# Kernel optimization log

Hardware: AMD Instinct MI355X
Metric: run time of the kernel (lower is better)

The kernel has to match this reference:

```python
import jax, jax.numpy as jnp
import numpy as np

N_NODES = 40000
N_EDGES = 640000
IN_CH = 128
OUT_CH = 128
NUM_RBF = 64


def setup_inputs() -> dict:
    key = jax.random.key(0)
    ks = jax.random.split(key, 8)
    x = jax.random.normal(ks[0], (N_NODES, IN_CH), dtype=jnp.float32)
    edge_index = jax.random.randint(ks[1], (2, N_EDGES), 0, N_NODES, dtype=jnp.int64)
    edge_rbf = jax.random.uniform(ks[2], (N_EDGES, NUM_RBF), dtype=jnp.float32)
    s1 = 1.0 / np.sqrt(NUM_RBF)
    s2 = 1.0 / np.sqrt(OUT_CH)
    sl = 1.0 / np.sqrt(IN_CH)
    W1 = jax.random.normal(ks[3], (NUM_RBF, OUT_CH), dtype=jnp.float32) * s1
    b1 = jnp.zeros((OUT_CH,), dtype=jnp.float32)
    W2 = jax.random.normal(ks[4], (OUT_CH, OUT_CH), dtype=jnp.float32) * s2
    b2 = jnp.zeros((OUT_CH,), dtype=jnp.float32)
    Wl = jax.random.normal(ks[5], (IN_CH, OUT_CH), dtype=jnp.float32) * sl
    bl = jnp.zeros((OUT_CH,), dtype=jnp.float32)
    return {"x": x, "edge_index": edge_index, "edge_rbf": edge_rbf,
            "W1": W1, "b1": b1, "W2": W2, "b2": b2, "Wl": Wl, "bl": bl}


def reference(x, edge_index, edge_rbf, W1, b1, W2, b2, Wl, bl):
    # filter_net: Linear -> ReLU -> Linear on edge RBF features  [E, OUT_CH]
    weight = jnp.maximum(edge_rbf @ W1 + b1, 0.0) @ W2 + b2
    # node linear projection  [N, OUT_CH]
    h = x @ Wl + bl
    row, col = edge_index[0], edge_index[1]
    # gather source node features, modulate by continuous filter
    msg = h[col] * weight  # [E, OUT_CH]
    # scatter-sum messages onto destination nodes
    out = jax.ops.segment_sum(msg, row, num_segments=x.shape[0])
    return out
```

## Files before the change

kernel.cpp:

```cpp
#include <hip/hip_runtime.h>


#define N_NODES 40000
#define N_EDGES 640000
#define IN_CH 128
#define OUT_CH 128
#define NUM_RBF 64

#define TILE_M 64
#define NTILES (N_EDGES / TILE_M)
#define NB_NODE (N_NODES / TILE_M)
#define RBF_STR 72
#define T_STR 136
#define HV_STR 136
#define W1_STR 72
#define W2_STR 136
#define NSCB ((N_NODES + 255) / 256)
#define EDGE_GRID 1024
#define K1_GRID 1024
#define ZC_BLOCKS 32

typedef __attribute__((ext_vector_type(8))) short bf16x8;
typedef __attribute__((ext_vector_type(16))) float f32x16;

__device__ __forceinline__ unsigned short f2bf(float f) {
  unsigned u = __float_as_uint(f);
  return (unsigned short)((u + 0x7FFFu + ((u >> 16) & 1u)) >> 16);
}
__device__ __forceinline__ float bf2f(unsigned short s) {
  return __uint_as_float(((unsigned)s) << 16);
}

__global__ __launch_bounds__(256) void k1_kernel(
    const float* __restrict__ x, const float* __restrict__ Wl,
    const float* __restrict__ bl, unsigned short* __restrict__ hbf,
    int* __restrict__ count, float* __restrict__ outp) {
  __shared__ __align__(16) char pool[IN_CH * W2_STR * 2];
  const int bid = blockIdx.x;
  const int t = threadIdx.x;

  if (bid >= NB_NODE) {
    if (bid < NB_NODE + ZC_BLOCKS) {
      if (count) {
        int4 z = {0, 0, 0, 0};
        for (int i = (bid - NB_NODE) * 256 + t; i < N_NODES / 4;
             i += ZC_BLOCKS * 256)
          ((int4*)count)[i] = z;
      }
    } else {
      if (outp) {
        float4 z = {0.f, 0.f, 0.f, 0.f};
        const int nb = K1_GRID - NB_NODE - ZC_BLOCKS;
        for (int i = (bid - NB_NODE - ZC_BLOCKS) * 256 + t;
             i < N_NODES * OUT_CH / 4; i += nb * 256)
          ((float4*)outp)[i] = z;
      }
    }
    return;
  }

  const int lane = t & 63;
  const int l31 = lane & 31;
  const int lhalf = lane >> 5;
  const int wv = t >> 6;
  const int nbase = wv * 32 + l31;

  {
    unsigned short* sWT = (unsigned short*)pool;
    const int k2 = t >> 1;
    const int d0 = (t & 1) * 64;
#pragma unroll
    for (int i = 0; i < 16; ++i) {
      float4 v = *(const float4*)(Wl + k2 * OUT_CH + d0 + 4 * i);
      sWT[(d0 + 4 * i + 0) * W2_STR + k2] = f2bf(v.x);
      sWT[(d0 + 4 * i + 1) * W2_STR + k2] = f2bf(v.y);
      sWT[(d0 + 4 * i + 2) * W2_STR + k2] = f2bf(v.z);
      sWT[(d0 + 4 * i + 3) * W2_STR + k2] = f2bf(v.w);
    }
  }
  __syncthreads();
  bf16x8 BW[8];
  {
    const unsigned short* sWT = (const unsigned short*)pool;
#pragma unroll
    for (int kk = 0; kk < 8; ++kk)
      BW[kk] = *(const bf16x8*)&sWT[nbase * W2_STR + kk * 16 + lhalf * 8];
  }
  const float blv = bl[nbase];
  __syncthreads();

  const int rbase = bid * TILE_M;
  unsigned short* sX = (unsigned short*)pool;
  {
    const int m = t >> 2;
    const int c0 = (t & 3) * 32;
    const float* src = x + (size_t)(rbase + m) * IN_CH + c0;
#pragma unroll
    for (int i = 0; i < 8; ++i) {
      float4 v = *(const float4*)(src + 4 * i);
      ushort4 p;
      p.x = f2bf(v.x); p.y = f2bf(v.y); p.z = f2bf(v.z); p.w = f2bf(v.w);
      *(ushort4*)&sX[m * T_STR + c0 + 4 * i] = p;
    }
  }
  __syncthreads();
#pragma unroll
  for (int mt = 0; mt < 2; ++mt) {
    f32x16 acc = {0.f, 0.f, 0.f, 0.f, 0.f, 0.f, 0.f, 0.f,
                  0.f, 0.f, 0.f, 0.f, 0.f, 0.f, 0.f, 0.f};
#pragma unroll
    for (int kk = 0; kk < 8; ++kk) {
      bf16x8 A = *(const bf16x8*)&sX[(mt * 32 + l31) * T_STR + kk * 16 + lhalf * 8];
      acc = __builtin_amdgcn_mfma_f32_32x32x16_bf16(A, BW[kk], acc, 0, 0, 0);
    }
#pragma unroll
    for (int r = 0; r < 16; ++r) {
      const int rowm = mt * 32 + (r & 3) + 8 * (r >> 2) + 4 * lhalf;
      hbf[(size_t)(rbase + rowm) * OUT_CH + nbase] = f2bf(acc[r] + blv);
    }
  }
}

__global__ void hist_kernel(const int* __restrict__ rowI, int* __restrict__ count,
                            unsigned long long* __restrict__ status) {
  if (blockIdx.x == 0 && threadIdx.x < NSCB) status[threadIdx.x] = 0ULL;
  int e = blockIdx.x * 256 + threadIdx.x;
  if (e < N_EDGES) atomicAdd(&count[rowI[e]], 1);
}

__global__ __launch_bounds__(256) void scan_kernel(
    const int* __restrict__ count, unsigned long long* __restrict__ status,
    int* __restrict__ cursor) {
  __shared__ int s[256];
  __shared__ int wsum[4];
  const int t = threadIdx.x;
  const int b = blockIdx.x;
  const int i = b * 256 + t;
  const int v = (i < N_NODES) ? count[i] : 0;
  s[t] = v;
  __syncthreads();
  for (int off = 1; off < 256; off <<= 1) {
    int u = (t >= off) ? s[t - off] : 0;
    __syncthreads();
    s[t] += u;
    __syncthreads();
  }
  if (t == 255)
    __hip_atomic_store(&status[b], (1ULL << 32) | (unsigned)s[255],
                       __ATOMIC_RELEASE, __HIP_MEMORY_SCOPE_AGENT);
  int contrib = 0;
  if (t < b) {
    unsigned long long sv;
    do {
      sv = __hip_atomic_load(&status[t], __ATOMIC_ACQUIRE,
                             __HIP_MEMORY_SCOPE_AGENT);
    } while (!(sv >> 32));
    contrib = (int)(unsigned)sv;
  }
  for (int o = 32; o > 0; o >>= 1) contrib += __shfl_down(contrib, o, 64);
  if ((t & 63) == 0) wsum[t >> 6] = contrib;
  __syncthreads();
  const int boffv = wsum[0] + wsum[1] + wsum[2] + wsum[3];
  if (i < N_NODES) cursor[i] = boffv + s[t] - v;
}

__global__ void scatter_kernel(const int* __restrict__ rowI,
                               const int* __restrict__ colI,
                               int* __restrict__ cursor,
                               unsigned long long* __restrict__ packed) {
  int e = blockIdx.x * 256 + threadIdx.x;
  if (e < N_EDGES) {
    const int r = rowI[e];
    const int c = colI[e];
    const int p = atomicAdd(&cursor[r], 1);
    packed[p] = ((unsigned long long)r << 36) | ((unsigned long long)c << 20) |
                (unsigned)e;
  }
}

__global__ __launch_bounds__(256, 3) void edge_fused_kernel(
    const unsigned long long* __restrict__ packed, const float* __restrict__ rbf,
    const float* __restrict__ W1, const float* __restrict__ b1,
    const float* __restrict__ W2, const float* __restrict__ b2,
    const unsigned short* __restrict__ hbf, float* __restrict__ outp) {
  __shared__ __align__(16) char pool[IN_CH * W2_STR * 2];

  unsigned short* sHv = (unsigned short*)pool;
  unsigned short* sT = (unsigned short*)pool;
  unsigned short* sRbf = (unsigned short*)(pool + TILE_M * HV_STR * 2);
  int* sAux = (int*)(pool + TILE_M * HV_STR * 2 + TILE_M * RBF_STR * 2);

  const int t = threadIdx.x;
  const int lane = t & 63;
  const int l31 = lane & 31;
  const int lhalf = lane >> 5;
  const int wv = t >> 6;
  const int nbase = wv * 32 + l31;

  {
    unsigned short* sW1T = (unsigned short*)pool;
    const int k = t >> 2;
    const int c0 = (t & 3) * 32;
#pragma unroll
    for (int i = 0; i < 8; ++i) {
      float4 v = *(const float4*)(W1 + k * OUT_CH + c0 + 4 * i);
      sW1T[(c0 + 4 * i + 0) * W1_STR + k] = f2bf(v.x);
      sW1T[(c0 + 4 * i + 1) * W1_STR + k] = f2bf(v.y);
      sW1T[(c0 + 4 * i + 2) * W1_STR + k] = f2bf(v.z);
      sW1T[(c0 + 4 * i + 3) * W1_STR + k] = f2bf(v.w);
    }
  }
  __syncthreads();
  bf16x8 B1[4];
  {
    const unsigned short* sW1T = (const unsigned short*)pool;
#pragma unroll
    for (int kk = 0; kk < 4; ++kk)
      B1[kk] = *(const bf16x8*)&sW1T[nbase * W1_STR + kk * 16 + lhalf * 8];
  }
  __syncthreads();
  {
    unsigned short* sW2T = (unsigned short*)pool;
    const int k2 = t >> 1;
    const int d0 = (t & 1) * 64;
#pragma unroll
    for (int i = 0; i < 16; ++i) {
      float4 v = *(const float4*)(W2 + k2 * OUT_CH + d0 + 4 * i);
      sW2T[(d0 + 4 * i + 0) * W2_STR + k2] = f2bf(v.x);
      sW2T[(d0 + 4 * i + 1) * W2_STR + k2] = f2bf(v.y);
      sW2T[(d0 + 4 * i + 2) * W2_STR + k2] = f2bf(v.z);
      sW2T[(d0 + 4 * i + 3) * W2_STR + k2] = f2bf(v.w);
    }
  }
  __syncthreads();
  bf16x8 B2[8];
  {
    const unsigned short* sW2T = (const unsigned short*)pool;
#pragma unroll
    for (int kk = 0; kk < 8; ++kk)
      B2[kk] = *(const bf16x8*)&sW2T[nbase * W2_STR + kk * 16 + lhalf * 8];
  }
  const float b1v = b1[nbase];
  const float b2v = b2[nbase];

  const int m4 = t >> 2;
  const int kq = (t & 3) * 16;
  const int rrow = t >> 4;
  const int c8 = (t & 15) * 8;

  float4 rb0, rb1, rb2, rb3;
  uint4 hq0, hq1, hq2, hq3;
  int auxv = 0;

#define PREFETCH(EB)                                                          \
  do {                                                                        \
    const unsigned long long pkm = packed[(EB) + m4];                         \
    const float* psrc = rbf + (size_t)(pkm & 0xFFFFFu) * NUM_RBF + kq;        \
    rb0 = *(const float4*)(psrc + 0);                                         \
    rb1 = *(const float4*)(psrc + 4);                                         \
    rb2 = *(const float4*)(psrc + 8);                                         \
    rb3 = *(const float4*)(psrc + 12);                                        \
    hq0 = *(const uint4*)(hbf +                                               \
        (size_t)((packed[(EB) + 0 + rrow] >> 20) & 0xFFFFu) * OUT_CH + c8);   \
    hq1 = *(const uint4*)(hbf +                                               \
        (size_t)((packed[(EB) + 16 + rrow] >> 20) & 0xFFFFu) * OUT_CH + c8);  \
    hq2 = *(const uint4*)(hbf +                                               \
        (size_t)((packed[(EB) + 32 + rrow] >> 20) & 0xFFFFu) * OUT_CH + c8);  \
    hq3 = *(const uint4*)(hbf +                                               \
        (size_t)((packed[(EB) + 48 + rrow] >> 20) & 0xFFFFu) * OUT_CH + c8);  \
    if (t < TILE_M) auxv = (int)(packed[(EB) + t] >> 36);                     \
  } while (0)

  int tile = blockIdx.x;
  if (tile < NTILES) PREFETCH(tile * TILE_M);

  for (; tile < NTILES; tile += gridDim.x) {
    __syncthreads();

    {
      ushort4 p;
      p.x = f2bf(rb0.x); p.y = f2bf(rb0.y); p.z = f2bf(rb0.z); p.w = f2bf(rb0.w);
      *(ushort4*)&sRbf[m4 * RBF_STR + kq + 0] = p;
      p.x = f2bf(rb1.x); p.y = f2bf(rb1.y); p.z = f2bf(rb1.z); p.w = f2bf(rb1.w);
      *(ushort4*)&sRbf[m4 * RBF_STR + kq + 4] = p;
      p.x = f2bf(rb2.x); p.y = f2bf(rb2.y); p.z = f2bf(rb2.z); p.w = f2bf(rb2.w);
      *(ushort4*)&sRbf[m4 * RBF_STR + kq + 8] = p;
      p.x = f2bf(rb3.x); p.y = f2bf(rb3.y); p.z = f2bf(rb3.z); p.w = f2bf(rb3.w);
      *(ushort4*)&sRbf[m4 * RBF_STR + kq + 12] = p;
    }
    *(uint4*)&sHv[(rrow + 0) * HV_STR + c8] = hq0;
    *(uint4*)&sHv[(rrow + 16) * HV_STR + c8] = hq1;
    *(uint4*)&sHv[(rrow + 32) * HV_STR + c8] = hq2;
    *(uint4*)&sHv[(rrow + 48) * HV_STR + c8] = hq3;
    if (t < TILE_M) sAux[t] = auxv;
    __syncthreads();

    const int tn = tile + gridDim.x;
    if (tn < NTILES) PREFETCH(tn * TILE_M);

    float hv[2][16];
#pragma unroll
    for (int mt = 0; mt < 2; ++mt)
#pragma unroll
      for (int r = 0; r < 16; ++r) {
        const int rowm = mt * 32 + (r & 3) + 8 * (r >> 2) + 4 * lhalf;
        hv[mt][r] = bf2f(sHv[rowm * HV_STR + nbase]);
      }
    __syncthreads();

#pragma unroll
    for (int mt = 0; mt < 2; ++mt) {
      f32x16 acc = {0.f, 0.f, 0.f, 0.f, 0.f, 0.f, 0.f, 0.f,
                    0.f, 0.f, 0.f, 0.f, 0.f, 0.f, 0.f, 0.f};
#pragma unroll
      for (int kk = 0; kk < 4; ++kk) {
        bf16x8 A = *(const bf16x8*)&sRbf[(mt * 32 + l31) * RBF_STR + kk * 16 + lhalf * 8];
        acc = __builtin_amdgcn_mfma_f32_32x32x16_bf16(A, B1[kk], acc, 0, 0, 0);
      }
#pragma unroll
      for (int r = 0; r < 16; ++r) {
        const int rowm = (r & 3) + 8 * (r >> 2) + 4 * lhalf;
        float v = acc[r] + b1v;
        v = v > 0.f ? v : 0.f;
        sT[(mt * 32 + rowm) * T_STR + nbase] = f2bf(v);
      }
    }
    __syncthreads();

    float sum = 0.f;
    int curd = -1;
#pragma unroll
    for (int mt = 0; mt < 2; ++mt) {
      f32x16 acc = {0.f, 0.f, 0.f, 0.f, 0.f, 0.f, 0.f, 0.f,
                    0.f, 0.f, 0.f, 0.f, 0.f, 0.f, 0.f, 0.f};
#pragma unroll
      for (int kk = 0; kk < 8; ++kk) {
        bf16x8 A = *(const bf16x8*)&sT[(mt * 32 + l31) * T_STR + kk * 16 + lhalf * 8];
        acc = __builtin_amdgcn_mfma_f32_32x32x16_bf16(A, B2[kk], acc, 0, 0, 0);
      }
#pragma unroll
      for (int r = 0; r < 16; ++r) {
        const int rowm = mt * 32 + (r & 3) + 8 * (r >> 2) + 4 * lhalf;
        const float m = hv[mt][r] * (acc[r] + b2v);
        const int d = sAux[rowm];
        if (d != curd) {
          if (curd >= 0) atomicAdd(&outp[(size_t)curd * OUT_CH + nbase], sum);
          curd = d;
          sum = m;
        } else {
          sum += m;
        }
      }
    }
    atomicAdd(&outp[(size_t)curd * OUT_CH + nbase], sum);
  }
#undef PREFETCH
}

__global__ __launch_bounds__(256, 3) void edge_atomic_kernel(
    const int* __restrict__ eidx, const float* __restrict__ rbf,
    const float* __restrict__ W1, const float* __restrict__ b1,
    const float* __restrict__ W2, const float* __restrict__ b2,
    const unsigned short* __restrict__ hbf, float* __restrict__ outp) {
  __shared__ __align__(16) char pool[IN_CH * W2_STR * 2];

  unsigned short* sHv = (unsigned short*)pool;
  unsigned short* sT = (unsigned short*)pool;
  unsigned short* sRbf = (unsigned short*)(pool + TILE_M * HV_STR * 2);
  int* sAux = (int*)(pool + TILE_M * HV_STR * 2 + TILE_M * RBF_STR * 2);

  const int t = threadIdx.x;
  const int lane = t & 63;
  const int l31 = lane & 31;
  const int lhalf = lane >> 5;
  const int wv = t >> 6;
  const int nbase = wv * 32 + l31;

  {
    unsigned short* sW1T = (unsigned short*)pool;
    const int k = t >> 2;
    const int c0 = (t & 3) * 32;
#pragma unroll
    for (int i = 0; i < 8; ++i) {
      float4 v = *(const float4*)(W1 + k * OUT_CH + c0 + 4 * i);
      sW1T[(c0 + 4 * i + 0) * W1_STR + k] = f2bf(v.x);
      sW1T[(c0 + 4 * i + 1) * W1_STR + k] = f2bf(v.y);
      sW1T[(c0 + 4 * i + 2) * W1_STR + k] = f2bf(v.z);
      sW1T[(c0 + 4 * i + 3) * W1_STR + k] = f2bf(v.w);
    }
  }
  __syncthreads();
  bf16x8 B1[4];
  {
    const unsigned short* sW1T = (const unsigned short*)pool;
#pragma unroll
    for (int kk = 0; kk < 4; ++kk)
      B1[kk] = *(const bf16x8*)&sW1T[nbase * W1_STR + kk * 16 + lhalf * 8];
  }
  __syncthreads();
  {
    unsigned short* sW2T = (unsigned short*)pool;
    const int k2 = t >> 1;
    const int d0 = (t & 1) * 64;
#pragma unroll
    for (int i = 0; i < 16; ++i) {
      float4 v = *(const float4*)(W2 + k2 * OUT_CH + d0 + 4 * i);
      sW2T[(d0 + 4 * i + 0) * W2_STR + k2] = f2bf(v.x);
      sW2T[(d0 + 4 * i + 1) * W2_STR + k2] = f2bf(v.y);
      sW2T[(d0 + 4 * i + 2) * W2_STR + k2] = f2bf(v.z);
      sW2T[(d0 + 4 * i + 3) * W2_STR + k2] = f2bf(v.w);
    }
  }
  __syncthreads();
  bf16x8 B2[8];
  {
    const unsigned short* sW2T = (const unsigned short*)pool;
#pragma unroll
    for (int kk = 0; kk < 8; ++kk)
      B2[kk] = *(const bf16x8*)&sW2T[nbase * W2_STR + kk * 16 + lhalf * 8];
  }
  const float b1v = b1[nbase];
  const float b2v = b2[nbase];

  const int* rowI = eidx;
  const int* colI = eidx + N_EDGES;

  for (int tile = blockIdx.x; tile < NTILES; tile += gridDim.x) {
    const int ebase = tile * TILE_M;
    __syncthreads();
    {
      const int m = t >> 2;
      const int kq = (t & 3) * 16;
      const float* src = rbf + (size_t)(ebase + m) * NUM_RBF + kq;
#pragma unroll
      for (int i = 0; i < 4; ++i) {
        float4 v = *(const float4*)(src + 4 * i);
        ushort4 p;
        p.x = f2bf(v.x); p.y = f2bf(v.y); p.z = f2bf(v.z); p.w = f2bf(v.w);
        *(ushort4*)&sRbf[m * RBF_STR + kq + 4 * i] = p;
      }
#pragma unroll
      for (int i = 0; i < 4; ++i) {
        const int chunk = t + 256 * i;
        const int row = chunk >> 4;
        const int c8 = (chunk & 15) * 8;
        const int col = colI[ebase + row];
        *(uint4*)&sHv[row * HV_STR + c8] =
            *(const uint4*)(hbf + (size_t)col * OUT_CH + c8);
      }
      if (t < TILE_M) sAux[t] = rowI[ebase + t];
    }
    __syncthreads();

    float hv[2][16];
#pragma unroll
    for (int mt = 0; mt < 2; ++mt)
#pragma unroll
      for (int r = 0; r < 16; ++r) {
        const int rowm = mt * 32 + (r & 3) + 8 * (r >> 2) + 4 * lhalf;
        hv[mt][r] = bf2f(sHv[rowm * HV_STR + nbase]);
      }
    __syncthreads();

#pragma unroll
    for (int mt = 0; mt < 2; ++mt) {
      f32x16 acc = {0.f, 0.f, 0.f, 0.f, 0.f, 0.f, 0.f, 0.f,
                    0.f, 0.f, 0.f, 0.f, 0.f, 0.f, 0.f, 0.f};
#pragma unroll
      for (int kk = 0; kk < 4; ++kk) {
        bf16x8 A = *(const bf16x8*)&sRbf[(mt * 32 + l31) * RBF_STR + kk * 16 + lhalf * 8];
        acc = __builtin_amdgcn_mfma_f32_32x32x16_bf16(A, B1[kk], acc, 0, 0, 0);
      }
#pragma unroll
      for (int r = 0; r < 16; ++r) {
        const int rowm = (r & 3) + 8 * (r >> 2) + 4 * lhalf;
        float v = acc[r] + b1v;
        v = v > 0.f ? v : 0.f;
        sT[(mt * 32 + rowm) * T_STR + nbase] = f2bf(v);
      }
    }
    __syncthreads();

    float sum = 0.f;
    int curd = -1;
#pragma unroll
    for (int mt = 0; mt < 2; ++mt) {
      f32x16 acc = {0.f, 0.f, 0.f, 0.f, 0.f, 0.f, 0.f, 0.f,
                    0.f, 0.f, 0.f, 0.f, 0.f, 0.f, 0.f, 0.f};
#pragma unroll
      for (int kk = 0; kk < 8; ++kk) {
        bf16x8 A = *(const bf16x8*)&sT[(mt * 32 + l31) * T_STR + kk * 16 + lhalf * 8];
        acc = __builtin_amdgcn_mfma_f32_32x32x16_bf16(A, B2[kk], acc, 0, 0, 0);
      }
#pragma unroll
      for (int r = 0; r < 16; ++r) {
        const int rowm = mt * 32 + (r & 3) + 8 * (r >> 2) + 4 * lhalf;
        const float m = hv[mt][r] * (acc[r] + b2v);
        const int d = sAux[rowm];
        if (d != curd) {
          if (curd >= 0) atomicAdd(&outp[(size_t)curd * OUT_CH + nbase], sum);
          curd = d;
          sum = m;
        } else {
          sum += m;
        }
      }
    }
    atomicAdd(&outp[(size_t)curd * OUT_CH + nbase], sum);
  }
}

extern "C" void kernel_launch(void* const* d_in, const int* in_sizes, int n_in,
                              void* d_out, int out_size, void* d_ws, size_t ws_size,
                              hipStream_t stream) {
  const float* x    = (const float*)d_in[0];
  const int*   eidx = (const int*)d_in[1];
  const float* rbf  = (const float*)d_in[2];
  const float* W1   = (const float*)d_in[3];
  const float* b1   = (const float*)d_in[4];
  const float* W2   = (const float*)d_in[5];
  const float* b2   = (const float*)d_in[6];
  const float* Wl   = (const float*)d_in[7];
  const float* bl   = (const float*)d_in[8];
  float* out = (float*)d_out;

  char* ws = (char*)d_ws;
  const size_t HBF_B = (size_t)N_NODES * OUT_CH * 2;
  const size_t PK_B = (size_t)N_EDGES * 8;
  const size_t CNT_B = (size_t)N_NODES * 4;
  const size_t ST_B = 1280;
  const size_t need = HBF_B + PK_B + 2 * CNT_B + ST_B + 64;

  size_t off = 0;
  unsigned short* hbf = (unsigned short*)(ws + off); off += HBF_B;
  unsigned long long* packed = (unsigned long long*)(ws + off); off += PK_B;
  int* count  = (int*)(ws + off); off += CNT_B;
  int* cursor = (int*)(ws + off); off += CNT_B;
  unsigned long long* status = (unsigned long long*)(ws + off); off += ST_B;

  const int* rowI = eidx;
  const int* colI = eidx + N_EDGES;

  if (ws_size >= need) {
    k1_kernel<<<K1_GRID, 256, 0, stream>>>(x, Wl, bl, hbf, count, out);
    hist_kernel<<<(N_EDGES + 255) / 256, 256, 0, stream>>>(rowI, count, status);
    scan_kernel<<<NSCB, 256, 0, stream>>>(count, status, cursor);
    scatter_kernel<<<(N_EDGES + 255) / 256, 256, 0, stream>>>(
        rowI, colI, cursor, packed);
    edge_fused_kernel<<<EDGE_GRID, 256, 0, stream>>>(
        packed, rbf, W1, b1, W2, b2, hbf, out);
  } else {
    hipMemsetAsync(out, 0, (size_t)N_NODES * OUT_CH * sizeof(float), stream);
    k1_kernel<<<NB_NODE, 256, 0, stream>>>(x, Wl, bl, hbf, nullptr, nullptr);
    edge_atomic_kernel<<<EDGE_GRID, 256, 0, stream>>>(
        eidx, rbf, W1, b1, W2, b2, hbf, out);
  }
}
```

Measured before the change: 418.8 us.

## Fold histogram into node-projection kernel and split packed edge keys into arrays

```diff
diff --git a/kernel.cpp b/kernel.cpp
--- a/kernel.cpp
+++ b/kernel.cpp
@@ -9,7 +9,7 @@
 
 #define TILE_M 64
 #define NTILES (N_EDGES / TILE_M)
-#define NB_NODE (N_NODES / TILE_M)
+#define NB_NODE (N_NODES / 64)
 #define RBF_STR 72
 #define T_STR 136
 #define HV_STR 136
@@ -18,7 +18,6 @@
 #define NSCB ((N_NODES + 255) / 256)
 #define EDGE_GRID 1024
 #define K1_GRID 1024
-#define ZC_BLOCKS 32
 
 typedef __attribute__((ext_vector_type(8))) short bf16x8;
 typedef __attribute__((ext_vector_type(16))) float f32x16;
@@ -34,27 +33,23 @@
 __global__ __launch_bounds__(256) void k1_kernel(
     const float* __restrict__ x, const float* __restrict__ Wl,
     const float* __restrict__ bl, unsigned short* __restrict__ hbf,
-    int* __restrict__ count, float* __restrict__ outp) {
+    const int* __restrict__ rowI, int* __restrict__ count,
+    float* __restrict__ outp) {
   __shared__ __align__(16) char pool[IN_CH * W2_STR * 2];
   const int bid = blockIdx.x;
   const int t = threadIdx.x;
 
   if (bid >= NB_NODE) {
-    if (bid < NB_NODE + ZC_BLOCKS) {
-      if (count) {
-        int4 z = {0, 0, 0, 0};
-        for (int i = (bid - NB_NODE) * 256 + t; i < N_NODES / 4;
-             i += ZC_BLOCKS * 256)
-          ((int4*)count)[i] = z;
-      }
-    } else {
-      if (outp) {
-        float4 z = {0.f, 0.f, 0.f, 0.f};
-        const int nb = K1_GRID - NB_NODE - ZC_BLOCKS;
-        for (int i = (bid - NB_NODE - ZC_BLOCKS) * 256 + t;
-             i < N_NODES * OUT_CH / 4; i += nb * 256)
-          ((float4*)outp)[i] = z;
-      }
+    const int nb = K1_GRID - NB_NODE;
+    if (outp) {
+      float4 z = {0.f, 0.f, 0.f, 0.f};
+      for (int i = (bid - NB_NODE) * 256 + t; i < N_NODES * OUT_CH / 4;
+           i += nb * 256)
+        ((float4*)outp)[i] = z;
+    }
+    if (count) {
+      for (int e = (bid - NB_NODE) * 256 + t; e < N_EDGES; e += nb * 256)
+        atomicAdd(&count[rowI[e]], 1);
     }
     return;
   }
@@ -89,7 +84,7 @@
   const float blv = bl[nbase];
   __syncthreads();
 
-  const int rbase = bid * TILE_M;
+  const int rbase = bid * 64;
   unsigned short* sX = (unsigned short*)pool;
   {
     const int m = t >> 2;
@@ -119,13 +114,6 @@
       hbf[(size_t)(rbase + rowm) * OUT_CH + nbase] = f2bf(acc[r] + blv);
     }
   }
-}
-
-__global__ void hist_kernel(const int* __restrict__ rowI, int* __restrict__ count,
-                            unsigned long long* __restrict__ status) {
-  if (blockIdx.x == 0 && threadIdx.x < NSCB) status[threadIdx.x] = 0ULL;
-  int e = blockIdx.x * 256 + threadIdx.x;
-  if (e < N_EDGES) atomicAdd(&count[rowI[e]], 1);
 }
 
 __global__ __launch_bounds__(256) void scan_kernel(
@@ -167,22 +155,24 @@
 __global__ void scatter_kernel(const int* __restrict__ rowI,
                                const int* __restrict__ colI,
                                int* __restrict__ cursor,
-                               unsigned long long* __restrict__ packed) {
+                               int* __restrict__ eperm, int* __restrict__ dsts,
+                               int* __restrict__ cols) {
   int e = blockIdx.x * 256 + threadIdx.x;
   if (e < N_EDGES) {
     const int r = rowI[e];
-    const int c = colI[e];
     const int p = atomicAdd(&cursor[r], 1);
-    packed[p] = ((unsigned long long)r << 36) | ((unsigned long long)c << 20) |
-                (unsigned)e;
-  }
-}
-
-__global__ __launch_bounds__(256, 3) void edge_fused_kernel(
-    const unsigned long long* __restrict__ packed, const float* __restrict__ rbf,
+    eperm[p] = e;
+    dsts[p] = r;
+    cols[p] = colI[e];
+  }
+}
+
+__global__ __launch_bounds__(256, 4) void edge_fused_kernel(
+    const int* __restrict__ eperm, const float* __restrict__ rbf,
     const float* __restrict__ W1, const float* __restrict__ b1,
     const float* __restrict__ W2, const float* __restrict__ b2,
-    const unsigned short* __restrict__ hbf, float* __restrict__ outp) {
+    const unsigned short* __restrict__ hbf, const int* __restrict__ dsts,
+    const int* __restrict__ cols, float* __restrict__ outp) {
   __shared__ __align__(16) char pool[IN_CH * W2_STR * 2];
 
   unsigned short* sHv = (unsigned short*)pool;
@@ -245,36 +235,22 @@
 
   const int m4 = t >> 2;
   const int kq = (t & 3) * 16;
-  const int rrow = t >> 4;
-  const int c8 = (t & 15) * 8;
 
   float4 rb0, rb1, rb2, rb3;
-  uint4 hq0, hq1, hq2, hq3;
-  int auxv = 0;
-
-#define PREFETCH(EB)                                                          \
-  do {                                                                        \
-    const unsigned long long pkm = packed[(EB) + m4];                         \
-    const float* psrc = rbf + (size_t)(pkm & 0xFFFFFu) * NUM_RBF + kq;        \
-    rb0 = *(const float4*)(psrc + 0);                                         \
-    rb1 = *(const float4*)(psrc + 4);                                         \
-    rb2 = *(const float4*)(psrc + 8);                                         \
-    rb3 = *(const float4*)(psrc + 12);                                        \
-    hq0 = *(const uint4*)(hbf +                                               \
-        (size_t)((packed[(EB) + 0 + rrow] >> 20) & 0xFFFFu) * OUT_CH + c8);   \
-    hq1 = *(const uint4*)(hbf +                                               \
-        (size_t)((packed[(EB) + 16 + rrow] >> 20) & 0xFFFFu) * OUT_CH + c8);  \
-    hq2 = *(const uint4*)(hbf +                                               \
-        (size_t)((packed[(EB) + 32 + rrow] >> 20) & 0xFFFFu) * OUT_CH + c8);  \
-    hq3 = *(const uint4*)(hbf +                                               \
-        (size_t)((packed[(EB) + 48 + rrow] >> 20) & 0xFFFFu) * OUT_CH + c8);  \
-    if (t < TILE_M) auxv = (int)(packed[(EB) + t] >> 36);                     \
+#define ISSUE_RBF(EB)                                                   \
+  do {                                                                  \
+    const int ep_ = eperm[(EB) + m4];                                   \
+    const float* ps_ = rbf + (size_t)ep_ * NUM_RBF + kq;                \
+    rb0 = *(const float4*)(ps_ + 0);                                    \
+    rb1 = *(const float4*)(ps_ + 4);                                    \
+    rb2 = *(const float4*)(ps_ + 8);                                    \
+    rb3 = *(const float4*)(ps_ + 12);                                   \
   } while (0)
 
-  int tile = blockIdx.x;
-  if (tile < NTILES) PREFETCH(tile * TILE_M);
-
-  for (; tile < NTILES; tile += gridDim.x) {
+  ISSUE_RBF(blockIdx.x * TILE_M);
+
+  for (int tile = blockIdx.x; tile < NTILES; tile += gridDim.x) {
+    const int ebase = tile * TILE_M;
     __syncthreads();
 
     {
@@ -287,16 +263,18 @@
       *(ushort4*)&sRbf[m4 * RBF_STR + kq + 8] = p;
       p.x = f2bf(rb3.x); p.y = f2bf(rb3.y); p.z = f2bf(rb3.z); p.w = f2bf(rb3.w);
       *(ushort4*)&sRbf[m4 * RBF_STR + kq + 12] = p;
-    }
-    *(uint4*)&sHv[(rrow + 0) * HV_STR + c8] = hq0;
-    *(uint4*)&sHv[(rrow + 16) * HV_STR + c8] = hq1;
-    *(uint4*)&sHv[(rrow + 32) * HV_STR + c8] = hq2;
-    *(uint4*)&sHv[(rrow + 48) * HV_STR + c8] = hq3;
-    if (t < TILE_M) sAux[t] = auxv;
-    __syncthreads();
-
-    const int tn = tile + gridDim.x;
-    if (tn < NTILES) PREFETCH(tn * TILE_M);
+#pragma unroll
+      for (int i = 0; i < 4; ++i) {
+        const int chunk = t + 256 * i;
+        const int row = chunk >> 4;
+        const int c8 = (chunk & 15) * 8;
+        const int col = cols[ebase + row];
+        *(uint4*)&sHv[row * HV_STR + c8] =
+            *(const uint4*)(hbf + (size_t)col * OUT_CH + c8);
+      }
+      if (t < TILE_M) sAux[t] = dsts[ebase + t];
+    }
+    __syncthreads();
 
     float hv[2][16];
 #pragma unroll
@@ -326,6 +304,9 @@
       }
     }
     __syncthreads();
+
+    const int tn = tile + gridDim.x;
+    if (tn < NTILES) ISSUE_RBF(tn * TILE_M);
 
     float sum = 0.f;
     int curd = -1;
@@ -354,10 +335,10 @@
     }
     atomicAdd(&outp[(size_t)curd * OUT_CH + nbase], sum);
   }
-#undef PREFETCH
-}
-
-__global__ __launch_bounds__(256, 3) void edge_atomic_kernel(
+#undef ISSUE_RBF
+}
+
+__global__ __launch_bounds__(256, 4) void edge_atomic_kernel(
     const int* __restrict__ eidx, const float* __restrict__ rbf,
     const float* __restrict__ W1, const float* __restrict__ b1,
     const float* __restrict__ W2, const float* __restrict__ b2,
@@ -526,32 +507,35 @@
 
   char* ws = (char*)d_ws;
   const size_t HBF_B = (size_t)N_NODES * OUT_CH * 2;
-  const size_t PK_B = (size_t)N_EDGES * 8;
+  const size_t EP_B = (size_t)N_EDGES * 4;
   const size_t CNT_B = (size_t)N_NODES * 4;
   const size_t ST_B = 1280;
-  const size_t need = HBF_B + PK_B + 2 * CNT_B + ST_B + 64;
+  const size_t need = HBF_B + 3 * EP_B + 2 * CNT_B + ST_B + 64;
 
   size_t off = 0;
   unsigned short* hbf = (unsigned short*)(ws + off); off += HBF_B;
-  unsigned long long* packed = (unsigned long long*)(ws + off); off += PK_B;
-  int* count  = (int*)(ws + off); off += CNT_B;
+  int* eperm = (int*)(ws + off); off += EP_B;
+  int* dsts  = (int*)(ws + off); off += EP_B;
+  int* cols  = (int*)(ws + off); off += EP_B;
+  int* count = (int*)(ws + off); off += CNT_B;
+  unsigned long long* status = (unsigned long long*)(ws + off); off += ST_B;
   int* cursor = (int*)(ws + off); off += CNT_B;
-  unsigned long long* status = (unsigned long long*)(ws + off); off += ST_B;
 
   const int* rowI = eidx;
   const int* colI = eidx + N_EDGES;
 
   if (ws_size >= need) {
-    k1_kernel<<<K1_GRID, 256, 0, stream>>>(x, Wl, bl, hbf, count, out);
-    hist_kernel<<<(N_EDGES + 255) / 256, 256, 0, stream>>>(rowI, count, status);
+    hipMemsetAsync(count, 0, CNT_B + ST_B, stream);
+    k1_kernel<<<K1_GRID, 256, 0, stream>>>(x, Wl, bl, hbf, rowI, count, out);
     scan_kernel<<<NSCB, 256, 0, stream>>>(count, status, cursor);
     scatter_kernel<<<(N_EDGES + 255) / 256, 256, 0, stream>>>(
-        rowI, colI, cursor, packed);
+        rowI, colI, cursor, eperm, dsts, cols);
     edge_fused_kernel<<<EDGE_GRID, 256, 0, stream>>>(
-        packed, rbf, W1, b1, W2, b2, hbf, out);
+        eperm, rbf, W1, b1, W2, b2, hbf, dsts, cols, out);
   } else {
     hipMemsetAsync(out, 0, (size_t)N_NODES * OUT_CH * sizeof(float), stream);
-    k1_kernel<<<NB_NODE, 256, 0, stream>>>(x, Wl, bl, hbf, nullptr, nullptr);
+    k1_kernel<<<NB_NODE, 256, 0, stream>>>(x, Wl, bl, hbf, rowI, nullptr,
+                                           nullptr);
     edge_atomic_kernel<<<EDGE_GRID, 256, 0, stream>>>(
         eidx, rbf, W1, b1, W2, b2, hbf, out);
   }
```

Result: slower. 445.6 us (+6.4%).
